# Kernel tuning notes

Hardware: AMD Instinct MI355X
Metric: run time of the kernel (lower is better)

The kernel has to match this reference:

```python
import jax, jax.numpy as jnp
import numpy as np

N_EMBED = 384
BLOCK_SIZE = 256
HEAD_SIZE = 64
B, T = 256, 256


def setup_inputs() -> dict:
    key = jax.random.key(0)
    k1, k2, k3, k4 = jax.random.split(key, 4)
    x = jax.random.normal(k1, (B, T, N_EMBED), dtype=jnp.float32)
    Wq = jax.random.normal(k2, (N_EMBED, HEAD_SIZE), dtype=jnp.float32) * (N_EMBED ** -0.5)
    Wk = jax.random.normal(k3, (N_EMBED, HEAD_SIZE), dtype=jnp.float32) * (N_EMBED ** -0.5)
    Wv = jax.random.normal(k4, (N_EMBED, HEAD_SIZE), dtype=jnp.float32) * (N_EMBED ** -0.5)
    return {"x": x, "Wq": Wq, "Wk": Wk, "Wv": Wv}


def reference(x, Wq, Wk, Wv):
    Bb, Tt, C = x.shape
    q = jnp.einsum("btc,ch->bth", x, Wq)
    k = jnp.einsum("btc,ch->bth", x, Wk)
    v = jnp.einsum("btc,ch->bth", x, Wv)
    # NOTE: original scales by C**-0.5 where C = n_embed (384), not head_size
    scale = jnp.asarray(C, x.dtype) ** -0.5
    wei = jnp.einsum("bqh,bkh->bqk", q, k) * scale  # [B, T, T]
    causal = jnp.tril(jnp.ones((Tt, Tt), dtype=bool))
    wei = jnp.where(causal, wei, -jnp.inf)
    wei = jax.nn.softmax(wei, axis=-1)
    out = jnp.einsum("bqk,bkh->bqh", wei, v)
    return out
```

## Files before the change

kernel.cpp:

```cpp
#include <hip/hip_runtime.h>
#include <hip/hip_bf16.h>
#include <math.h>

#define BB   256
#define TT   256
#define CIN  384
#define HS   64

#define QSCL ((float)(0.051031036307982884 * 1.4426950408889634))

typedef __attribute__((ext_vector_type(8))) short short8;
typedef __attribute__((ext_vector_type(4))) float floatx4;
typedef __attribute__((ext_vector_type(4))) float fx4;

__device__ inline short bf16bits(float f) {
    union { __hip_bfloat16 h; short s; } u;
    u.h = __float2bfloat16(f);
    return u.s;
}

__device__ inline short8 cvt8(const fx4& f0, const fx4& f1) {
    union { __hip_bfloat162 h[4]; short8 s8; } u;
    u.h[0] = __float22bfloat162_rn(make_float2(f0.x, f0.y));
    u.h[1] = __float22bfloat162_rn(make_float2(f0.z, f0.w));
    u.h[2] = __float22bfloat162_rn(make_float2(f1.x, f1.y));
    u.h[3] = __float22bfloat162_rn(make_float2(f1.z, f1.w));
    return u.s8;
}

__device__ inline fx4 ntload4(const float* p) {
    return __builtin_nontemporal_load((const fx4*)p);
}

__global__ __launch_bounds__(256) void prep_wtp(
    const float* __restrict__ Wq, const float* __restrict__ Wk,
    const float* __restrict__ Wv, short* __restrict__ WtP)
{
    const int idx  = blockIdx.x * 256 + threadIdx.x;
    const int j    = idx & 7;
    const int quad = (idx >> 3) & 3;
    const int l15  = (idx >> 5) & 15;
    int X          = idx >> 9;
    const int nt   = X % 6;  X /= 6;
    const int ks   = X & 1;  X >>= 1;
    const int s    = X % 6;  X /= 6;
    const int wn   = X;

    const int n  = wn * 96 + nt * 16 + l15;
    const int kk = s * 64 + ks * 32 + quad * 8 + j;
    const float* W = (n < 64) ? Wq : (n < 128) ? Wk : Wv;
    WtP[idx] = bf16bits(W[kk * 64 + (n & 63)]);
}

__global__ __launch_bounds__(512, 2) void qkv_gemm(
    const float* __restrict__ x, const short* __restrict__ WtP,
    short* __restrict__ qF, short* __restrict__ kF, short* __restrict__ vF)
{
    const int tid  = threadIdx.x;
    const int lane = tid & 63;
    const int w    = tid >> 6;
    const int l15  = lane & 15;
    const int quad = lane >> 4;
    const int kq   = quad * 8;
    const int crow = quad * 4;
    const int job  = blockIdx.x * 8 + w;
    const int laneoff = l15 * 32 + kq;

    const float* xr = x + (size_t)(job * 16 + l15) * 384 + kq;

    floatx4 acc[12] = {};

    fx4 c00 = ntload4(xr + 0);
    fx4 c01 = ntload4(xr + 4);
    fx4 c10 = ntload4(xr + 32);
    fx4 c11 = ntload4(xr + 36);

#pragma unroll
    for (int s = 0; s < 6; ++s) {
        const short8 af0 = cvt8(c00, c01);
        const short8 af1 = cvt8(c10, c11);
        if (s < 5) {
            c00 = ntload4(xr + (s + 1) * 64 + 0);
            c01 = ntload4(xr + (s + 1) * 64 + 4);
            c10 = ntload4(xr + (s + 1) * 64 + 32);
            c11 = ntload4(xr + (s + 1) * 64 + 36);
        }
#pragma unroll
        for (int q = 0; q < 4; ++q) {
            const int ks = q >> 1, h = q & 1;
            short8 bb[6];
#pragma unroll
            for (int nt = 0; nt < 6; ++nt)
                bb[nt] = *(const short8*)
                    &WtP[((((h * 6 + s) * 2 + ks) * 6 + nt) << 9) + laneoff];
            __builtin_amdgcn_sched_barrier(0);
            const short8 af = ks ? af1 : af0;
#pragma unroll
            for (int nt = 0; nt < 6; ++nt)
                acc[h * 6 + nt] = __builtin_amdgcn_mfma_f32_16x16x32_bf16(
                    af, bb[nt], acc[h * 6 + nt], 0, 0, 0);
        }
    }

    const int b = job >> 4;
    const int g = job & 15;
#pragma unroll
    for (int j = 0; j < 12; ++j) {
#pragma unroll
        for (int r = 0; r < 4; ++r) {
            const float av = acc[j][r];
            if (j < 4) {
                qF[(((b * 16 + g) * 2 + (j >> 1)) << 9)
                   + (crow + r) * 32 + (j & 1) * 16 + l15]
                    = bf16bits(av * QSCL);
            } else if (j < 8) {
                kF[(((b * 16 + g) * 2 + ((j - 4) >> 1)) << 9)
                   + (crow + r) * 32 + (j & 1) * 16 + l15]
                    = bf16bits(av);
            } else {
                vF[(((b * 4 + (j - 8)) * 8 + (g >> 1)) << 9)
                   + l15 * 32 + (g & 1) * 16 + crow + r]
                    = bf16bits(av);
            }
        }
    }
}

__global__ __launch_bounds__(256, 4) void attn(
    const short* __restrict__ qF, const short* __restrict__ kF,
    const short* __restrict__ vF, float* __restrict__ out)
{
    __shared__ short Ps[4 * 16 * 40];

    const int tid  = threadIdx.x;
    const int lane = tid & 63;
    const int wv   = tid >> 6;
    const int l15  = lane & 15;
    const int quad = lane >> 4;
    const int kq   = quad * 8;
    const int crow = quad * 4;

    const int b = blockIdx.x >> 1;
    const int p = (blockIdx.x & 1) * 4 + wv;

#pragma unroll
    for (int gi = 0; gi < 2; ++gi) {
        const int g  = gi ? (15 - p) : p;
        const int r0 = g * 16;

        const short8 aq0 = *(const short8*)
            &qF[(((b * 16 + g) * 2 + 0) << 9) + l15 * 32 + kq];
        const short8 aq1 = *(const short8*)
            &qF[(((b * 16 + g) * 2 + 1) << 9) + l15 * 32 + kq];

        float lsum[4] = {0.f, 0.f, 0.f, 0.f};
        floatx4 O[4] = {};

        const int nch = (r0 + 47) >> 5;
        for (int c = 0; c < nch; ++c) {
            const int cb = c * 32;

            floatx4 st[2];
#pragma unroll
            for (int t = 0; t < 2; ++t) {
                const short8 b0 = *(const short8*)
                    &kF[(((b * 16 + (2 * c + t)) * 2 + 0) << 9) + l15 * 32 + kq];
                const short8 b1 = *(const short8*)
                    &kF[(((b * 16 + (2 * c + t)) * 2 + 1) << 9) + l15 * 32 + kq];
                floatx4 z = {};
                z = __builtin_amdgcn_mfma_f32_16x16x32_bf16(aq0, b0, z, 0, 0, 0);
                z = __builtin_amdgcn_mfma_f32_16x16x32_bf16(aq1, b1, z, 0, 0, 0);
                st[t] = z;
            }

#pragma unroll
            for (int t = 0; t < 2; ++t)
#pragma unroll
                for (int r = 0; r < 4; ++r) {
                    const int key  = cb + t * 16 + l15;
                    const int qrow = r0 + crow + r;
                    float pp = __builtin_amdgcn_exp2f(st[t][r]);
                    pp = (key <= qrow) ? pp : 0.f;
                    lsum[r] += pp;
                    Ps[wv * 640 + (crow + r) * 40 + t * 16 + l15] = bf16bits(pp);
                }

            asm volatile("s_waitcnt lgkmcnt(0)" ::: "memory");

            const short8 pa = *(const short8*)&Ps[wv * 640 + l15 * 40 + kq];
#pragma unroll
            for (int nb = 0; nb < 4; ++nb) {
                const short8 bv = *(const short8*)
                    &vF[(((b * 4 + nb) * 8 + c) << 9) + l15 * 32 + kq];
                O[nb] = __builtin_amdgcn_mfma_f32_16x16x32_bf16(pa, bv, O[nb], 0, 0, 0);
            }
        }

#pragma unroll
        for (int off = 1; off < 16; off <<= 1)
#pragma unroll
            for (int r = 0; r < 4; ++r)
                lsum[r] += __shfl_xor(lsum[r], off, 16);

        float inv[4];
#pragma unroll
        for (int r = 0; r < 4; ++r) inv[r] = 1.f / lsum[r];
#pragma unroll
        for (int nb = 0; nb < 4; ++nb)
#pragma unroll
            for (int r = 0; r < 4; ++r)
                out[(size_t)(b * 256 + r0 + crow + r) * 64 + nb * 16 + l15]
                    = O[nb][r] * inv[r];
    }
}

extern "C" void kernel_launch(void* const* d_in, const int* in_sizes, int n_in,
                              void* d_out, int out_size, void* d_ws, size_t ws_size,
                              hipStream_t stream)
{
    const float* x  = (const float*)d_in[0];
    const float* Wq = (const float*)d_in[1];
    const float* Wk = (const float*)d_in[2];
    const float* Wv = (const float*)d_in[3];
    float* out = (float*)d_out;

    short* WtP = (short*)d_ws;
    short* qF  = WtP + 73728;
    short* kF  = qF + 4194304;
    short* vF  = kF + 4194304;

    prep_wtp<<<(192 * 384) / 256, 256, 0, stream>>>(Wq, Wk, Wv, WtP);
    qkv_gemm<<<512, 512, 0, stream>>>(x, WtP, qF, kF, vF);
    attn<<<512, 256, 0, stream>>>(qF, kF, vF, out);
}
```

Before: 198.2 us.

## Give each attention wave one query tile and prefetch K/V per chunk

The attention kernel now gives each wave a single 16-row query tile, and the grid doubles to 1024 blocks. Before, each wave handled two tiles paired for causal balance. Within each key chunk, all K and V fragments are loaded up front, ahead of the QK MFMAs, with a scheduling barrier so memory latency overlaps compute. Launch attributes change to amdgpu_waves_per_eu hints on both the GEMM and attention kernels to steer register allocation and occupancy. The cost is uneven causal work across waves in a block, and more registers held by the prefetched fragments.

```diff
diff --git a/kernel.cpp b/kernel.cpp
--- a/kernel.cpp
+++ b/kernel.cpp
@@ -52,7 +52,9 @@
     WtP[idx] = bf16bits(W[kk * 64 + (n & 63)]);
 }
 
-__global__ __launch_bounds__(512, 2) void qkv_gemm(
+__global__ void
+__attribute__((amdgpu_flat_work_group_size(512, 512), amdgpu_waves_per_eu(4, 4)))
+qkv_gemm(
     const float* __restrict__ x, const short* __restrict__ WtP,
     short* __restrict__ qF, short* __restrict__ kF, short* __restrict__ vF)
 {
@@ -126,7 +128,9 @@
     }
 }
 
-__global__ __launch_bounds__(256, 4) void attn(
+__global__ void
+__attribute__((amdgpu_flat_work_group_size(256, 256), amdgpu_waves_per_eu(4, 8)))
+attn(
     const short* __restrict__ qF, const short* __restrict__ kF,
     const short* __restrict__ vF, float* __restrict__ out)
 {
@@ -140,78 +144,86 @@
     const int kq   = quad * 8;
     const int crow = quad * 4;
 
-    const int b = blockIdx.x >> 1;
-    const int p = (blockIdx.x & 1) * 4 + wv;
-
-#pragma unroll
-    for (int gi = 0; gi < 2; ++gi) {
-        const int g  = gi ? (15 - p) : p;
-        const int r0 = g * 16;
-
-        const short8 aq0 = *(const short8*)
-            &qF[(((b * 16 + g) * 2 + 0) << 9) + l15 * 32 + kq];
-        const short8 aq1 = *(const short8*)
-            &qF[(((b * 16 + g) * 2 + 1) << 9) + l15 * 32 + kq];
-
-        float lsum[4] = {0.f, 0.f, 0.f, 0.f};
-        floatx4 O[4] = {};
-
-        const int nch = (r0 + 47) >> 5;
-        for (int c = 0; c < nch; ++c) {
-            const int cb = c * 32;
-
-            floatx4 st[2];
-#pragma unroll
-            for (int t = 0; t < 2; ++t) {
-                const short8 b0 = *(const short8*)
-                    &kF[(((b * 16 + (2 * c + t)) * 2 + 0) << 9) + l15 * 32 + kq];
-                const short8 b1 = *(const short8*)
-                    &kF[(((b * 16 + (2 * c + t)) * 2 + 1) << 9) + l15 * 32 + kq];
-                floatx4 z = {};
-                z = __builtin_amdgcn_mfma_f32_16x16x32_bf16(aq0, b0, z, 0, 0, 0);
-                z = __builtin_amdgcn_mfma_f32_16x16x32_bf16(aq1, b1, z, 0, 0, 0);
-                st[t] = z;
+    const int b = blockIdx.x >> 2;
+    const int g = wv * 4 + (blockIdx.x & 3);
+    const int r0 = g * 16;
+
+    const short8 aq0 = *(const short8*)
+        &qF[(((b * 16 + g) * 2 + 0) << 9) + l15 * 32 + kq];
+    const short8 aq1 = *(const short8*)
+        &qF[(((b * 16 + g) * 2 + 1) << 9) + l15 * 32 + kq];
+
+    float lsum[4] = {0.f, 0.f, 0.f, 0.f};
+    floatx4 O[4] = {};
+
+    const int nch = (r0 + 47) >> 5;
+    for (int c = 0; c < nch; ++c) {
+        const int cb = c * 32;
+
+        const short8 kb00 = *(const short8*)
+            &kF[(((b * 16 + (2 * c + 0)) * 2 + 0) << 9) + l15 * 32 + kq];
+        const short8 kb01 = *(const short8*)
+            &kF[(((b * 16 + (2 * c + 0)) * 2 + 1) << 9) + l15 * 32 + kq];
+        const short8 kb10 = *(const short8*)
+            &kF[(((b * 16 + (2 * c + 1)) * 2 + 0) << 9) + l15 * 32 + kq];
+        const short8 kb11 = *(const short8*)
+            &kF[(((b * 16 + (2 * c + 1)) * 2 + 1) << 9) + l15 * 32 + kq];
+        short8 bv[4];
+#pragma unroll
+        for (int nb = 0; nb < 4; ++nb)
+            bv[nb] = *(const short8*)
+                &vF[(((b * 4 + nb) * 8 + c) << 9) + l15 * 32 + kq];
+        __builtin_amdgcn_sched_barrier(0);
+
+        floatx4 st[2];
+        {
+            floatx4 z = {};
+            z = __builtin_amdgcn_mfma_f32_16x16x32_bf16(aq0, kb00, z, 0, 0, 0);
+            z = __builtin_amdgcn_mfma_f32_16x16x32_bf16(aq1, kb01, z, 0, 0, 0);
+            st[0] = z;
+        }
+        {
+            floatx4 z = {};
+            z = __builtin_amdgcn_mfma_f32_16x16x32_bf16(aq0, kb10, z, 0, 0, 0);
+            z = __builtin_amdgcn_mfma_f32_16x16x32_bf16(aq1, kb11, z, 0, 0, 0);
+            st[1] = z;
+        }
+
+#pragma unroll
+        for (int t = 0; t < 2; ++t)
+#pragma unroll
+            for (int r = 0; r < 4; ++r) {
+                const int key  = cb + t * 16 + l15;
+                const int qrow = r0 + crow + r;
+                float pp = __builtin_amdgcn_exp2f(st[t][r]);
+                pp = (key <= qrow) ? pp : 0.f;
+                lsum[r] += pp;
+                Ps[wv * 640 + (crow + r) * 40 + t * 16 + l15] = bf16bits(pp);
             }
 
-#pragma unroll
-            for (int t = 0; t < 2; ++t)
-#pragma unroll
-                for (int r = 0; r < 4; ++r) {
-                    const int key  = cb + t * 16 + l15;
-                    const int qrow = r0 + crow + r;
-                    float pp = __builtin_amdgcn_exp2f(st[t][r]);
-                    pp = (key <= qrow) ? pp : 0.f;
-                    lsum[r] += pp;
-                    Ps[wv * 640 + (crow + r) * 40 + t * 16 + l15] = bf16bits(pp);
-                }
-
-            asm volatile("s_waitcnt lgkmcnt(0)" ::: "memory");
-
-            const short8 pa = *(const short8*)&Ps[wv * 640 + l15 * 40 + kq];
-#pragma unroll
-            for (int nb = 0; nb < 4; ++nb) {
-                const short8 bv = *(const short8*)
-                    &vF[(((b * 4 + nb) * 8 + c) << 9) + l15 * 32 + kq];
-                O[nb] = __builtin_amdgcn_mfma_f32_16x16x32_bf16(pa, bv, O[nb], 0, 0, 0);
-            }
-        }
-
-#pragma unroll
-        for (int off = 1; off < 16; off <<= 1)
-#pragma unroll
-            for (int r = 0; r < 4; ++r)
-                lsum[r] += __shfl_xor(lsum[r], off, 16);
-
-        float inv[4];
-#pragma unroll
-        for (int r = 0; r < 4; ++r) inv[r] = 1.f / lsum[r];
+        asm volatile("s_waitcnt lgkmcnt(0)" ::: "memory");
+
+        const short8 pa = *(const short8*)&Ps[wv * 640 + l15 * 40 + kq];
 #pragma unroll
         for (int nb = 0; nb < 4; ++nb)
-#pragma unroll
-            for (int r = 0; r < 4; ++r)
-                out[(size_t)(b * 256 + r0 + crow + r) * 64 + nb * 16 + l15]
-                    = O[nb][r] * inv[r];
+            O[nb] = __builtin_amdgcn_mfma_f32_16x16x32_bf16(pa, bv[nb], O[nb], 0, 0, 0);
     }
+
+#pragma unroll
+    for (int off = 1; off < 16; off <<= 1)
+#pragma unroll
+        for (int r = 0; r < 4; ++r)
+            lsum[r] += __shfl_xor(lsum[r], off, 16);
+
+    float inv[4];
+#pragma unroll
+    for (int r = 0; r < 4; ++r) inv[r] = 1.f / lsum[r];
+#pragma unroll
+    for (int nb = 0; nb < 4; ++nb)
+#pragma unroll
+        for (int r = 0; r < 4; ++r)
+            out[(size_t)(b * 256 + r0 + crow + r) * 64 + nb * 16 + l15]
+                = O[nb][r] * inv[r];
 }
 
 extern "C" void kernel_launch(void* const* d_in, const int* in_sizes, int n_in,
@@ -231,5 +243,5 @@
 
     prep_wtp<<<(192 * 384) / 256, 256, 0, stream>>>(Wq, Wk, Wv, WtP);
     qkv_gemm<<<512, 512, 0, stream>>>(x, WtP, qF, kF, vF);
-    attn<<<512, 256, 0, stream>>>(qF, kF, vF, out);
-}
+    attn<<<1024, 256, 0, stream>>>(qF, kF, vF, out);
+}
```

New measurement: 198.0 us. No clear change (-0.1%).
